# Kernel tuning notes

Measured on AMD Instinct MI355X. Metric: run time of the kernel, lower is better.

Reference implementation:

```python
import jax, jax.numpy as jnp
import numpy as np
from jax import lax

N = 5000          # num atoms
E = 4             # num edge types
DIM_H = 128
VOCAB = 100       # num_atoms_vocab; embedding table has VOCAB+1 rows
T = 4             # max_time_steps


def setup_inputs() -> dict:
    key = jax.random.key(0)
    k1, k2, k3, k4 = jax.random.split(key, 4)
    atom_arr = jax.random.randint(k1, (N,), 0, VOCAB, dtype=jnp.int64 if jax.config.read('jax_enable_x64') else jnp.int32)
    adjs = jax.random.randint(k2, (E, N, N), 0, 2, dtype=jnp.int32)
    # learned parameters
    embedding = jax.random.normal(k3, (VOCAB + 1, DIM_H), dtype=jnp.float32) * 0.05
    limit = float(np.sqrt(6.0 / (DIM_H + DIM_H)))  # glorot uniform
    H_edges = jax.random.uniform(k4, (E, DIM_H, DIM_H), minval=-limit, maxval=limit, dtype=jnp.float32)
    return {
        "atom_arr": atom_arr,
        "adjs": adjs,
        "max_time_steps": T,
        "embedding": embedding,
        "H_edges": H_edges,
    }


def reference(atom_arr, adjs, max_time_steps, embedding, H_edges):
    # h_v^0 = embedding lookup, [N, H]
    h0 = embedding[atom_arr]
    # adjacency mask as float, [E, N, N]
    A = (adjs == 1).astype(h0.dtype)

    def step(h, _):
        # original: for each node v, edge type e: H_e @ sum_{u: adj[e,v,u]==1} h_u
        agg = jnp.einsum('evu,uh->evh', A, h)          # neighbor sum per edge type
        msg = jnp.einsum('eij,evj->vi', H_edges, agg)  # edge-type transform + sum over e
        h_new = jax.nn.sigmoid(h + msg)
        return h_new, h_new

    _, h_all = lax.scan(step, h0, None, length=max_time_steps)
    return h_all  # [T, N, H]
```

## Files before the change

kernel.cpp:

```cpp
#include <hip/hip_runtime.h>

#define NROW 5000
#define NPAD 5120
#define KW   80
#define KC   80
#define KZ   4
#define KCQ  20
#define HDIM 128
#define MTI  4
#define MROWS (MTI * 32)
#define FXS  4194304.0f
#define PART ((size_t)4 * NROW * HDIM)

typedef _Float16 f16x8 __attribute__((ext_vector_type(8)));
typedef float f32x16 __attribute__((ext_vector_type(16)));

__device__ __forceinline__ unsigned short f2h_int(int v) {
    union { _Float16 h; unsigned short u; } c;
    c.h = (_Float16)(float)v;
    return c.u;
}
__device__ __forceinline__ void fx_digits(float h, unsigned short& d1, unsigned short& d0) {
    int q = (int)rintf(h * FXS);
    d1 = f2h_int(q >> 11);
    d0 = f2h_int(q & 2047);
}

__device__ __forceinline__ size_t bt_idx(int kc, int pl, int kk, int half, int col, int j) {
    return (((((size_t)kc * 2 + pl) * 4 + kk) * 2 + half) * 128 + col) * 8 + j;
}

__global__ __launch_bounds__(256) void prep_atom_kernel(const unsigned int* __restrict__ atomw,
                                                        int* __restrict__ atomIdx) {
    __shared__ int s_is64;
    if (threadIdx.x == 0) {
        bool all0 = true, anynz = false;
        for (int j = 0; j < 64; ++j) {
            unsigned lo = atomw[2 * j], hi = atomw[2 * j + 1];
            all0 = all0 && (hi == 0u);
            anynz = anynz || (lo != 0u);
        }
        s_is64 = (all0 && anynz) ? 1 : 0;
    }
    __syncthreads();
    int v = blockIdx.x * 256 + threadIdx.x;
    if (v < NROW) atomIdx[v] = s_is64 ? (int)atomw[2 * v] : (int)atomw[v];
}

__global__ __launch_bounds__(256) void prep_pack_kernel(const int* __restrict__ adjs,
                                                        unsigned long long* __restrict__ packedR) {
    const int er = blockIdx.x;
    const int e = er / NPAD;
    const int r = er - e * NPAD;
    const int wave = threadIdx.x >> 6;
    const int lane = threadIdx.x & 63;
    const int* rowp = adjs + ((size_t)e * NROW + r) * NROW;
    unsigned long long* outp = packedR + ((size_t)e * NPAD + r) * KW;
    const bool rok = (r < NROW);
    for (int c = wave; c < KW; c += 4) {
        int u = c * 64 + lane;
        int val = (rok && u < NROW) ? rowp[u] : 0;
        unsigned long long m = __ballot(val == 1);
        if (lane == 0) outp[c] = m;
    }
}

__global__ __launch_bounds__(256) void prep_packT_kernel(const unsigned long long* __restrict__ packedR,
                                                         unsigned long long* __restrict__ packedT) {
    __shared__ unsigned long long slds[64][KW + 1];
    const int e = blockIdx.y;
    const int r0 = blockIdx.x * 64;
    const int tid = threadIdx.x;
#pragma unroll
    for (int p = 0; p < 20; ++p) {
        int idx = p * 256 + tid;
        int r = idx / KW;
        int c = idx - r * KW;
        slds[r][c] = packedR[((size_t)e * NPAD + r0 + r) * KW + c];
    }
    __syncthreads();
#pragma unroll
    for (int p = 0; p < 20; ++p) {
        int idx = p * 256 + tid;
        int kc = idx >> 6;
        int rr = idx & 63;
        packedT[((size_t)e * KC + kc) * NPAD + r0 + rr] = slds[rr][kc];
    }
}

__global__ __launch_bounds__(256) void prep_h0T_kernel(const int* __restrict__ atomIdx,
                                                       const float* __restrict__ emb,
                                                       unsigned short* __restrict__ hTt) {
    const int i = blockIdx.y;
    const int v = blockIdx.x * 256 + threadIdx.x;
    float val = 0.f;
    if (v < NROW) val = emb[(size_t)atomIdx[v] * HDIM + i];
    unsigned short d1, d0;
    fx_digits(val, d1, d0);
    const int kc = v >> 6, kk = (v >> 4) & 3, half = (v >> 3) & 1, j = v & 7;
    hTt[bt_idx(kc, 0, kk, half, i, j)] = d1;
    hTt[bt_idx(kc, 1, kk, half, i, j)] = d0;
}

__global__ __launch_bounds__(256) void prep_h0f_kernel(const int* __restrict__ atomIdx,
                                                       const float* __restrict__ emb,
                                                       float* __restrict__ h) {
    int idx = blockIdx.x * 256 + threadIdx.x;
    int v = idx >> 7, i = idx & 127;
    h[idx] = emb[(size_t)atomIdx[v] * HDIM + i];
}

__global__ __launch_bounds__(256) void prep_Ht_kernel(const float* __restrict__ H,
                                                      float* __restrict__ Htr) {
    int idx = blockIdx.x * 256 + threadIdx.x;
    int e = idx >> 14;
    int j = (idx >> 7) & 127;
    int i = idx & 127;
    Htr[idx] = H[((size_t)e * HDIM + i) * HDIM + j];
}

__global__ __launch_bounds__(256, 2) void gemm1_kernel(const unsigned long long* __restrict__ packedT,
                                                       const unsigned short* __restrict__ hTt,
                                                       float* __restrict__ agg) {
    const int m0 = blockIdx.x * MROWS;
    const int e = blockIdx.y;
    const int kz = blockIdx.z;
    const int tid = threadIdx.x;
    const int lane = tid & 63;
    const int wave = tid >> 6;
    const int l31 = lane & 31;
    const int l1 = lane >> 5;
    const int sh2 = l1 * 8;
    const int col = wave * 32 + l31;
    const int kc0 = kz * KCQ;

    f32x16 acc[2][MTI];
#pragma unroll
    for (int pl = 0; pl < 2; ++pl)
#pragma unroll
        for (int mt = 0; mt < MTI; ++mt) acc[pl][mt] = (f32x16)(0.f);

    const unsigned long long* ap = packedT + ((size_t)e * KC + kc0) * NPAD + m0 + l31;
    const _Float16* bp = (const _Float16*)hTt + (size_t)kc0 * 16384 +
                         (size_t)l1 * 1024 + (size_t)col * 8;

    for (int kc = 0; kc < KCQ; ++kc) {
        unsigned long long aw[MTI];
#pragma unroll
        for (int mt = 0; mt < MTI; ++mt) aw[mt] = ap[mt * 32];

        f16x8 bf[2][4];
#pragma unroll
        for (int pl = 0; pl < 2; ++pl)
#pragma unroll
            for (int kk = 0; kk < 4; ++kk)
                bf[pl][kk] = *(const f16x8*)(bp + pl * 8192 + kk * 2048);

        ap += NPAD;
        bp += 16384;

#pragma unroll
        for (int kk = 0; kk < 4; ++kk) {
#pragma unroll
            for (int mt = 0; mt < MTI; ++mt) {
                unsigned int w = (kk < 2) ? (unsigned int)aw[mt]
                                          : (unsigned int)(aw[mt] >> 32);
                unsigned int b = (w >> ((kk & 1) * 16 + sh2)) & 0xFFu;
                unsigned int y = b | (b << 15);
                union { unsigned int u[4]; f16x8 h; } Af;
#pragma unroll
                for (int q = 0; q < 4; ++q)
                    Af.u[q] = ((y >> (2 * q)) & 0x00010001u) * 0x3C00u;
#pragma unroll
                for (int pl = 0; pl < 2; ++pl)
                    acc[pl][mt] = __builtin_amdgcn_mfma_f32_32x32x16_f16(
                        Af.h, bf[pl][kk], acc[pl][mt], 0, 0, 0);
            }
        }
    }

    float* aggz = agg + (size_t)kz * PART;
#pragma unroll
    for (int mt = 0; mt < MTI; ++mt)
#pragma unroll
        for (int reg = 0; reg < 16; ++reg) {
            int row = (reg & 3) + 8 * (reg >> 2) + 4 * l1;
            int v = m0 + mt * 32 + row;
            if (v < NROW) {
                double d = (double)acc[0][mt][reg] * 2048.0 + (double)acc[1][mt][reg];
                aggz[((size_t)e * NROW + v) * HDIM + col] = (float)(d * (1.0 / 4194304.0));
            }
        }
}

__global__ __launch_bounds__(256) void gemm2_kernel(const float* __restrict__ agg,
                                                    const float* __restrict__ Htr,
                                                    float* __restrict__ hf,
                                                    float* __restrict__ outp,
                                                    unsigned short* __restrict__ hTt) {
    __shared__ float aggs[8][512];
    __shared__ unsigned short hs[2][128][8];
    const int tid = threadIdx.x;
    const int v0 = blockIdx.x * 8;

#pragma unroll
    for (int it = 0; it < 4; ++it) {
        int idx = it * 256 + tid;
        int r = idx >> 7;
        int c = (idx & 127) * 4;
        int e = c >> 7, j = c & 127;
        size_t o = ((size_t)e * NROW + (v0 + r)) * HDIM + j;
        float4 a0 = *(const float4*)&agg[o];
        float4 a1 = *(const float4*)&agg[PART + o];
        float4 a2 = *(const float4*)&agg[2 * PART + o];
        float4 a3 = *(const float4*)&agg[3 * PART + o];
        *(float4*)&aggs[r][c] = make_float4((a0.x + a1.x) + (a2.x + a3.x),
                                            (a0.y + a1.y) + (a2.y + a3.y),
                                            (a0.z + a1.z) + (a2.z + a3.z),
                                            (a0.w + a1.w) + (a2.w + a3.w));
    }
    __syncthreads();

    const int ip = tid & 63;
    const int vg = tid >> 6;
    const int i0 = ip * 2;

    float m[2][2][4];
#pragma unroll
    for (int r = 0; r < 2; ++r)
#pragma unroll
        for (int q = 0; q < 2; ++q)
#pragma unroll
            for (int k = 0; k < 4; ++k) m[r][q][k] = 0.f;

    const int rb = vg * 2;
    for (int cg = 0; cg < 128; ++cg) {
        int c = cg * 4;
        float4 q0 = *(const float4*)&aggs[rb][c];
        float4 q1 = *(const float4*)&aggs[rb + 1][c];
        float a0v[4] = {q0.x, q0.y, q0.z, q0.w};
        float a1v[4] = {q1.x, q1.y, q1.z, q1.w};
#pragma unroll
        for (int k = 0; k < 4; ++k) {
            float2 w = *(const float2*)&Htr[(size_t)(c + k) * HDIM + i0];
            m[0][0][k] += a0v[k] * w.x;
            m[0][1][k] += a0v[k] * w.y;
            m[1][0][k] += a1v[k] * w.x;
            m[1][1][k] += a1v[k] * w.y;
        }
    }

#pragma unroll
    for (int r = 0; r < 2; ++r) {
        int vr = rb + r;
        int v = v0 + vr;
        size_t o = (size_t)v * HDIM + i0;
        float2 hv = *(const float2*)&hf[o];
        float ms0 = (m[r][0][0] + m[r][0][1]) + (m[r][0][2] + m[r][0][3]);
        float ms1 = (m[r][1][0] + m[r][1][1]) + (m[r][1][2] + m[r][1][3]);
        float x0 = hv.x + ms0;
        float x1 = hv.y + ms1;
        float s0 = 1.0f / (1.0f + expf(-x0));
        float s1 = 1.0f / (1.0f + expf(-x1));
        *(float2*)&outp[o] = make_float2(s0, s1);
        *(float2*)&hf[o] = make_float2(s0, s1);
        unsigned short d1a, d0a, d1b, d0b;
        fx_digits(s0, d1a, d0a);
        fx_digits(s1, d1b, d0b);
        hs[0][i0][vr] = d1a;
        hs[1][i0][vr] = d0a;
        hs[0][i0 + 1][vr] = d1b;
        hs[1][i0 + 1][vr] = d0b;
    }
    __syncthreads();
    if (tid < 128) {
        const int kc = v0 >> 6, kk = (v0 >> 4) & 3, half = (v0 >> 3) & 1;
#pragma unroll
        for (int pl = 0; pl < 2; ++pl)
            *(uint4*)&hTt[bt_idx(kc, pl, kk, half, tid, 0)] = *(const uint4*)&hs[pl][tid][0];
    }
}

extern "C" void kernel_launch(void* const* d_in, const int* in_sizes, int n_in,
                              void* d_out, int out_size, void* d_ws, size_t ws_size,
                              hipStream_t stream) {
    const unsigned int* atomw = (const unsigned int*)d_in[0];
    const int* adjs = (const int*)d_in[1];
    const float* emb = (const float*)d_in[3];
    const float* H = (const float*)d_in[4];
    float* out = (float*)d_out;

    char* ws = (char*)d_ws;
    unsigned long long* packedT = (unsigned long long*)ws;
    size_t off = (size_t)4 * KC * NPAD * 8;
    unsigned short* hTt = (unsigned short*)(ws + off);
    off += (size_t)2 * KC * HDIM * 64 * 2;
    float* hf = (float*)(ws + off);
    off += (size_t)NROW * HDIM * 4;
    float* agg = (float*)(ws + off);
    off += (size_t)KZ * PART * 4;
    float* Htr = (float*)(ws + off);
    off += (size_t)4 * HDIM * HDIM * 4;
    int* atomIdx = (int*)(ws + off);
    off += (size_t)NROW * 4;
    off = (off + 255) & ~(size_t)255;
    unsigned long long* packedR = (unsigned long long*)(ws + off);
    off += (size_t)4 * NPAD * KW * 8;

    prep_atom_kernel<<<dim3((NROW + 255) / 256), 256, 0, stream>>>(atomw, atomIdx);
    prep_pack_kernel<<<dim3(4 * NPAD), 256, 0, stream>>>(adjs, packedR);
    prep_packT_kernel<<<dim3(NPAD / 64, 4), 256, 0, stream>>>(packedR, packedT);
    prep_h0T_kernel<<<dim3(NPAD / 256, HDIM), 256, 0, stream>>>(atomIdx, emb, hTt);
    prep_h0f_kernel<<<dim3(NROW * HDIM / 256), 256, 0, stream>>>(atomIdx, emb, hf);
    prep_Ht_kernel<<<dim3(4 * HDIM * HDIM / 256), 256, 0, stream>>>(H, Htr);

    for (int t = 0; t < 4; ++t) {
        gemm1_kernel<<<dim3(NPAD / MROWS, 4, KZ), 256, 0, stream>>>(packedT, hTt, agg);
        gemm2_kernel<<<dim3(NROW / 8), 256, 0, stream>>>(agg, Htr, hf,
                                                         out + (size_t)t * NROW * HDIM, hTt);
    }
}
```

Baseline: 1.019 ms.

## Double-buffer gemm1 B tiles in LDS via async global_load_lds

gemm1 now stages each B slab of hTt (32KB per kc step) into a double-buffered shared-memory array using global_load_lds, prefetching the next slab while computing the current one, and reads B fragments from LDS instead of directly from global memory. The aim is to hide global load latency and share B loads across waves. It uses 64KB of LDS per block, which may limit the two-blocks-per-CU occupancy target, and adds a barrier per iteration. The gemm2 inner loop also gets an unroll-4 pragma.

Measured after the change: 1.067 ms. 1.05x slower.

```diff
diff --git a/kernel.cpp b/kernel.cpp
--- a/kernel.cpp
+++ b/kernel.cpp
@@ -8,7 +8,6 @@
 #define KCQ  20
 #define HDIM 128
 #define MTI  4
-#define MROWS (MTI * 32)
 #define FXS  4194304.0f
 #define PART ((size_t)4 * NROW * HDIM)
 
@@ -122,7 +121,8 @@
 __global__ __launch_bounds__(256, 2) void gemm1_kernel(const unsigned long long* __restrict__ packedT,
                                                        const unsigned short* __restrict__ hTt,
                                                        float* __restrict__ agg) {
-    const int m0 = blockIdx.x * MROWS;
+    __shared__ _Float16 Bs[2][16384];
+    const int m0 = blockIdx.x * 128;
     const int e = blockIdx.y;
     const int kz = blockIdx.z;
     const int tid = threadIdx.x;
@@ -141,23 +141,37 @@
         for (int mt = 0; mt < MTI; ++mt) acc[pl][mt] = (f32x16)(0.f);
 
     const unsigned long long* ap = packedT + ((size_t)e * KC + kc0) * NPAD + m0 + l31;
-    const _Float16* bp = (const _Float16*)hTt + (size_t)kc0 * 16384 +
-                         (size_t)l1 * 1024 + (size_t)col * 8;
-
+    const char* bslab = (const char*)hTt + (size_t)kc0 * 32768;
+
+#define STAGE(BUF, KCV)                                                         \
+    {                                                                           \
+        const char* gs_ = bslab + (size_t)(KCV) * 32768;                        \
+        char* ls_ = (char*)&Bs[BUF][0] + (tid & 192) * 16;                      \
+        _Pragma("unroll") for (int c_ = 0; c_ < 8; ++c_)                        \
+            __builtin_amdgcn_global_load_lds(                                   \
+                (const unsigned int*)(gs_ + c_ * 4096 + tid * 16),              \
+                (unsigned int*)(ls_ + c_ * 4096), 16, 0, 0);                    \
+    }
+
+    STAGE(0, 0)
+    __syncthreads();
+
+    int cur = 0;
     for (int kc = 0; kc < KCQ; ++kc) {
         unsigned long long aw[MTI];
 #pragma unroll
         for (int mt = 0; mt < MTI; ++mt) aw[mt] = ap[mt * 32];
-
+        ap += NPAD;
+
+        if (kc + 1 < KCQ) STAGE(cur ^ 1, kc + 1)
+
+        const _Float16* bl = &Bs[cur][(size_t)l1 * 1024 + col * 8];
         f16x8 bf[2][4];
 #pragma unroll
         for (int pl = 0; pl < 2; ++pl)
 #pragma unroll
             for (int kk = 0; kk < 4; ++kk)
-                bf[pl][kk] = *(const f16x8*)(bp + pl * 8192 + kk * 2048);
-
-        ap += NPAD;
-        bp += 16384;
+                bf[pl][kk] = *(const f16x8*)(bl + (pl * 4 + kk) * 2048);
 
 #pragma unroll
         for (int kk = 0; kk < 4; ++kk) {
@@ -177,7 +191,10 @@
                         Af.h, bf[pl][kk], acc[pl][mt], 0, 0, 0);
             }
         }
-    }
+        __syncthreads();
+        cur ^= 1;
+    }
+#undef STAGE
 
     float* aggz = agg + (size_t)kz * PART;
 #pragma unroll
@@ -234,6 +251,7 @@
             for (int k = 0; k < 4; ++k) m[r][q][k] = 0.f;
 
     const int rb = vg * 2;
+#pragma unroll 4
     for (int cg = 0; cg < 128; ++cg) {
         int c = cg * 4;
         float4 q0 = *(const float4*)&aggs[rb][c];
@@ -315,7 +333,7 @@
     prep_Ht_kernel<<<dim3(4 * HDIM * HDIM / 256), 256, 0, stream>>>(H, Htr);
 
     for (int t = 0; t < 4; ++t) {
-        gemm1_kernel<<<dim3(NPAD / MROWS, 4, KZ), 256, 0, stream>>>(packedT, hTt, agg);
+        gemm1_kernel<<<dim3(NPAD / 128, 4, KZ), 256, 0, stream>>>(packedT, hTt, agg);
         gemm2_kernel<<<dim3(NROW / 8), 256, 0, stream>>>(agg, Htr, hf,
                                                          out + (size_t)t * NROW * HDIM, hTt);
     }
```
